# Kernel optimization log

Measured on AMD Instinct MI355X. Metric: run time of the kernel, lower is better.

The kernel has to match this reference:

```python
import jax, jax.numpy as jnp
import numpy as np

V_TH = 1.0
V_RESET = 0.0
BN_EPS = 1e-5

# Heaviside spike with ATan surrogate gradient (spikingjelly surrogate.ATan, alpha=2)
@jax.custom_vjp
def spike(x):
    return (x >= 0).astype(x.dtype)

def _spike_fwd(x):
    return spike(x), x

def _spike_bwd(x, g):
    alpha = 2.0
    sg = (alpha / 2.0) / (1.0 + (jnp.pi / 2.0 * alpha * x) ** 2)
    return (g * sg,)

spike.defvjp(_spike_fwd, _spike_bwd)


def lif_block(x, w, W, b, gamma, beta):
    """LTLIF (learnable tau, decay_input=False, hard reset) -> Linear -> BatchNorm1d.
    x: [T, B, C]"""
    inv_tau = jax.nn.sigmoid(w)  # 1/tau, learnable via w

    def step(v, xt):
        # decay_input=False charge: v = v - (v - v_reset)/tau + x_t
        v = v - (v - V_RESET) * inv_tau + xt
        s = spike(v - V_TH)
        v = (1.0 - s) * v + s * V_RESET  # hard reset
        return v, s

    v0 = jnp.full(x.shape[1:], V_RESET, dtype=x.dtype)
    _, spikes = jax.lax.scan(step, v0, x)  # spikes: [T, B, C]

    y = jnp.einsum('tbc,dc->tbd', spikes, W) + b  # Linear per step
    # BatchNorm1d in multi-step mode: stats over flattened (T*B) per channel
    mean = jnp.mean(y, axis=(0, 1))
    var = jnp.var(y, axis=(0, 1))
    y = (y - mean) * jax.lax.rsqrt(var + BN_EPS) * gamma + beta
    return y


def setup_inputs() -> dict:
    key = jax.random.key(0)
    ks = jax.random.split(key, 3)
    T, B, C = 128, 256, 512
    scale = 1.0 / np.sqrt(C)
    return {
        'x': jax.random.normal(ks[0], (T, B, C), jnp.float32),
        'w0': jnp.zeros((), jnp.float32),  # sigmoid(0)=0.5 => tau=2
        'W0': jax.random.normal(ks[1], (C, C), jnp.float32) * scale,
        'b0': jnp.zeros((C,), jnp.float32),
        'gamma0': jnp.ones((C,), jnp.float32),
        'beta0': jnp.zeros((C,), jnp.float32),
        'w1': jnp.zeros((), jnp.float32),
        'W1': jax.random.normal(ks[2], (C, C), jnp.float32) * scale,
        'b1': jnp.zeros((C,), jnp.float32),
        'gamma1': jnp.ones((C,), jnp.float32),
        'beta1': jnp.zeros((C,), jnp.float32),
    }


def reference(x, w0, W0, b0, gamma0, beta0, w1, W1, b1, gamma1, beta1):
    h = lif_block(x, w0, W0, b0, gamma0, beta0)   # process block (Dropout p=0 -> identity)
    h = lif_block(h, w1, W1, b1, gamma1, beta1)   # out block
    return h + x  # skip_connect=True
```

## Files before the change

kernel.cpp:

```cpp
#include <hip/hip_runtime.h>


typedef int i32x4 __attribute__((ext_vector_type(4)));

#define T_STEPS 128
#define BATCH   256
#define CH      512
#define BC      (BATCH * CH)
#define MROWS   (T_STEPS * BATCH)

__device__ __forceinline__ void llds16(const void* g, void* l) {
  __builtin_amdgcn_global_load_lds(
      (const __attribute__((address_space(1))) void*)g,
      (__attribute__((address_space(3))) void*)l, 16, 0, 0);
}

__global__ __launch_bounds__(256) void k_convw(const float* __restrict__ W0,
                                               const float* __restrict__ W1,
                                               signed char* __restrict__ WL0,
                                               signed char* __restrict__ WL1) {
  int b = blockIdx.x;
  const float* W = (b < 1024) ? W0 : W1;
  signed char* WL = (b < 1024) ? WL0 : WL1;
  int i = (b & 1023) * 256 + threadIdx.x;
  double z = (double)W[i] * 4294967296.0;
  z = fmin(fmax(z, -2147483647.0), 2147483647.0);
  int q = (int)llrint(z);
  int r = q;
  signed char l0 = (signed char)r; r = (r - l0) >> 8;
  signed char l1 = (signed char)r; r = (r - l1) >> 8;
  signed char l2 = (signed char)r; r = (r - l2) >> 8;
  signed char l3 = (signed char)r;
  WL[i]          = l0;
  WL[i + 262144] = l1;
  WL[i + 524288] = l2;
  WL[i + 786432] = l3;
}

__global__ __launch_bounds__(64) void k_lif1(const float* __restrict__ X,
                                             const float* __restrict__ wp,
                                             signed char* __restrict__ S) {
  int i = blockIdx.x * 64 + threadIdx.x;
  float om = 1.0f - 1.0f / (1.0f + expf(-wp[0]));
  float v = 0.0f;
  #pragma unroll 8
  for (int t = 0; t < T_STEPS; ++t) {
    float xt = X[(size_t)t * BC + i];
    v = v * om + xt;
    bool sp = (v >= 1.0f);
    S[(size_t)t * BC + i] = sp;
    v = sp ? 0.0f : v;
  }
}

__global__ __launch_bounds__(64) void k_lif2(const float* __restrict__ Y,
                                             const double* __restrict__ sA,
                                             const double* __restrict__ sB,
                                             const float* __restrict__ wp,
                                             signed char* __restrict__ S) {
  int i = blockIdx.x * 64 + threadIdx.x;
  int c = i & (CH - 1);
  double a = sA[c], b = sB[c];
  float om = 1.0f - 1.0f / (1.0f + expf(-wp[0]));
  float v = 0.0f;
  #pragma unroll 8
  for (int t = 0; t < T_STEPS; ++t) {
    float h = (float)((double)Y[(size_t)t * BC + i] * a + b);
    v = v * om + h;
    bool sp = (v >= 1.0f);
    S[(size_t)t * BC + i] = sp;
    v = sp ? 0.0f : v;
  }
}

__global__ __launch_bounds__(256) void k_gemm(const signed char* __restrict__ S,
                                              const signed char* __restrict__ WL,
                                              float* __restrict__ Y,
                                              double* __restrict__ sumP,
                                              double* __restrict__ sqP) {
  __shared__ __align__(16) signed char Bb[2][4][64 * 64];

  const int tid  = threadIdx.x;
  const int wid  = tid >> 6;
  const int lane = tid & 63;
  const int bid   = blockIdx.x;
  const int xcd   = bid & 7;
  const int local = bid >> 3;
  const int bn    = local & 7;
  const int bm    = xcd * 32 + (local >> 3);
  const int m0 = bm * 128, n0 = bn * 64;
  const int wm = wid >> 1, wn = wid & 1;
  const int lr = lane & 15, lg = lane >> 4;

  i32x4 acc[4][2][4] = {};

  auto STAGE = [&](int buf, int kt) {
    int row = tid >> 2, gl = tid & 3;
    int gg = gl ^ ((row >> 1) & 3);
    #pragma unroll
    for (int j = 0; j < 4; ++j)
      llds16(WL + (size_t)j * 262144 + (size_t)(n0 + row) * 512 + kt + gg * 16,
             (char*)Bb[buf][j] + wid * 1024);
  };

  const signed char* aP = S + (size_t)(m0 + wm * 64 + lr) * 512 + lg * 16;
  i32x4 a[2][4];

  STAGE(0, 0);
  #pragma unroll
  for (int m = 0; m < 4; ++m)
    a[0][m] = *(const i32x4*)(aP + m * 8192);

  #pragma unroll
  for (int i = 0; i < 8; ++i) {
    const int cur = i & 1;
    if (i < 7) {
      STAGE(cur ^ 1, (i + 1) * 64);
      #pragma unroll
      for (int m = 0; m < 4; ++m)
        a[cur ^ 1][m] = *(const i32x4*)(aP + m * 8192 + (i + 1) * 64);
    }
    if (i < 7) asm volatile("s_waitcnt vmcnt(8)" ::: "memory");
    else       asm volatile("s_waitcnt vmcnt(0)" ::: "memory");
    __builtin_amdgcn_s_barrier();
    asm volatile("" ::: "memory");

    i32x4 b[2][4];
    #pragma unroll
    for (int n = 0; n < 2; ++n) {
      int r = wn * 32 + n * 16 + lr;
      int g = lg ^ ((r >> 1) & 3);
      #pragma unroll
      for (int j = 0; j < 4; ++j)
        b[n][j] = *(const i32x4*)(Bb[cur][j] + r * 64 + g * 16);
    }
    __builtin_amdgcn_sched_barrier(0);

    __builtin_amdgcn_s_setprio(1);
    #pragma unroll
    for (int j = 0; j < 4; ++j)
      #pragma unroll
      for (int m = 0; m < 4; ++m)
        #pragma unroll
        for (int n = 0; n < 2; ++n)
          acc[m][n][j] = __builtin_amdgcn_mfma_i32_16x16x64_i8(
              a[cur][m], b[n][j], acc[m][n][j], 0, 0, 0);
    __builtin_amdgcn_s_setprio(0);

    asm volatile("s_waitcnt lgkmcnt(0)" ::: "memory");
    __builtin_amdgcn_s_barrier();
  }

  const int r0 = m0 + wm * 64 + lg * 4;
  const int cl = wn * 32 + lr;
  double s0 = 0, q0 = 0, s1 = 0, q1 = 0;
  #pragma unroll
  for (int m = 0; m < 4; ++m)
    #pragma unroll
    for (int n = 0; n < 2; ++n)
      #pragma unroll
      for (int q = 0; q < 4; ++q) {
        double yv = (((double)acc[m][n][3][q] * 256.0 + (double)acc[m][n][2][q]) * 256.0
                     + (double)acc[m][n][1][q]) * 256.0 + (double)acc[m][n][0][q];
        float yf = (float)(yv * 0x1p-32);
        Y[(size_t)(r0 + m * 16 + q) * 512 + n0 + cl + n * 16] = yf;
        double yd = (double)yf;
        if (n == 0) { s0 += yd; q0 += yd * yd; }
        else        { s1 += yd; q1 += yd * yd; }
      }
  s0 += __shfl_xor(s0, 16); s0 += __shfl_xor(s0, 32);
  q0 += __shfl_xor(q0, 16); q0 += __shfl_xor(q0, 32);
  s1 += __shfl_xor(s1, 16); s1 += __shfl_xor(s1, 32);
  q1 += __shfl_xor(q1, 16); q1 += __shfl_xor(q1, 32);

  double* shS = (double*)Bb[0][0];
  double* shQ = shS + 128;
  if (lane < 16) {
    shS[wm * 64 + cl]      = s0;  shQ[wm * 64 + cl]      = q0;
    shS[wm * 64 + cl + 16] = s1;  shQ[wm * 64 + cl + 16] = q1;
  }
  __syncthreads();
  if (tid < 64) {
    sumP[(size_t)(n0 + tid) * 256 + bm] = shS[tid] + shS[64 + tid];
    sqP [(size_t)(n0 + tid) * 256 + bm] = shQ[tid] + shQ[64 + tid];
  }
}

__global__ __launch_bounds__(256) void k_stats2(const double* __restrict__ sumP,
                                                const double* __restrict__ sqP,
                                                const float* __restrict__ gamma,
                                                const float* __restrict__ beta,
                                                double* __restrict__ sA,
                                                double* __restrict__ sB) {
  __shared__ double shS[256], shQ[256];
  int c = blockIdx.x;
  int t = threadIdx.x;
  shS[t] = sumP[(size_t)c * 256 + t];
  shQ[t] = sqP [(size_t)c * 256 + t];
  __syncthreads();
  for (int w = 128; w >= 1; w >>= 1) {
    if (t < w) { shS[t] += shS[t + w]; shQ[t] += shQ[t + w]; }
    __syncthreads();
  }
  if (t == 0) {
    const double invN = 1.0 / 32768.0;
    double mean = shS[0] * invN;
    double var  = shQ[0] * invN - mean * mean;
    double rstd = rsqrt(var + 1e-5);
    double a = (double)gamma[c] * rstd;
    sA[c] = a;
    sB[c] = (double)beta[c] - mean * a;
  }
}

__global__ __launch_bounds__(256) void k_final(float* __restrict__ Y,
                                               const float* __restrict__ X,
                                               const double* __restrict__ sA,
                                               const double* __restrict__ sB) {
  size_t i = (size_t)blockIdx.x * 256 + threadIdx.x;
  int c0 = (int)((i * 4) & (CH - 1));
  float4 y = ((const float4*)Y)[i];
  float4 x = ((const float4*)X)[i];
  float4 o;
  o.x = (float)((double)y.x * sA[c0 + 0] + sB[c0 + 0] + (double)x.x);
  o.y = (float)((double)y.y * sA[c0 + 1] + sB[c0 + 1] + (double)x.y);
  o.z = (float)((double)y.z * sA[c0 + 2] + sB[c0 + 2] + (double)x.z);
  o.w = (float)((double)y.w * sA[c0 + 3] + sB[c0 + 3] + (double)x.w);
  ((float4*)Y)[i] = o;
}

extern "C" void kernel_launch(void* const* d_in, const int* in_sizes, int n_in,
                              void* d_out, int out_size, void* d_ws, size_t ws_size,
                              hipStream_t stream) {
  (void)in_sizes; (void)n_in; (void)out_size; (void)ws_size;

  const float* x   = (const float*)d_in[0];
  const float* w0  = (const float*)d_in[1];
  const float* W0  = (const float*)d_in[2];
  const float* g0  = (const float*)d_in[4];
  const float* be0 = (const float*)d_in[5];
  const float* w1  = (const float*)d_in[6];
  const float* W1  = (const float*)d_in[7];
  const float* g1  = (const float*)d_in[9];
  const float* be1 = (const float*)d_in[10];
  float* Y = (float*)d_out;

  char* ws = (char*)d_ws;
  signed char* WL0  = (signed char*)(ws + 0x0000000);
  signed char* WL1  = (signed char*)(ws + 0x0100000);
  signed char* spk  = (signed char*)(ws + 0x0200000);
  double*      sumP = (double*)(ws + 0x1200000);
  double*      sqP  = (double*)(ws + 0x1300000);
  double*      sA   = (double*)(ws + 0x1400000);
  double*      sB   = (double*)(ws + 0x1402000);

  k_convw<<<2048, 256, 0, stream>>>(W0, W1, WL0, WL1);

  k_lif1 <<<BC / 64, 64, 0, stream>>>(x, w0, spk);
  k_gemm <<<(MROWS / 128) * (CH / 64), 256, 0, stream>>>(spk, WL0, Y, sumP, sqP);
  k_stats2<<<512, 256, 0, stream>>>(sumP, sqP, g0, be0, sA, sB);

  k_lif2 <<<BC / 64, 64, 0, stream>>>(Y, sA, sB, w1, spk);
  k_gemm <<<(MROWS / 128) * (CH / 64), 256, 0, stream>>>(spk, WL1, Y, sumP, sqP);
  k_stats2<<<512, 256, 0, stream>>>(sumP, sqP, g1, be1, sA, sB);

  k_final<<<(MROWS * CH) / (4 * 256), 256, 0, stream>>>(Y, x, sA, sB);
}
```

Before: 217.5 us.

## Drop LDS staging in int8 GEMM; each wave loads its own tiles directly

The GEMM kernel no longer stages weight tiles through shared memory with global_load_lds and barriers. Each wave now computes a 64x16 output tile and loads both A and B fragments straight from global memory into registers, with double buffering. The block tile shrinks to 64 rows, so the grid doubles, and the partial BN statistics are written per wave with a 512-wide stride that the stats kernel folds. This removes LDS traffic and barrier stalls and adds occupancy hints, at the cost of less data reuse and more redundant global and L2 reads of the spike and weight tiles.

```diff
diff --git a/kernel.cpp b/kernel.cpp
--- a/kernel.cpp
+++ b/kernel.cpp
@@ -8,12 +8,6 @@
 #define CH      512
 #define BC      (BATCH * CH)
 #define MROWS   (T_STEPS * BATCH)
-
-__device__ __forceinline__ void llds16(const void* g, void* l) {
-  __builtin_amdgcn_global_load_lds(
-      (const __attribute__((address_space(1))) void*)g,
-      (__attribute__((address_space(3))) void*)l, 16, 0, 0);
-}
 
 __global__ __launch_bounds__(256) void k_convw(const float* __restrict__ W0,
                                                const float* __restrict__ W1,
@@ -73,66 +67,46 @@
   }
 }
 
-__global__ __launch_bounds__(256) void k_gemm(const signed char* __restrict__ S,
-                                              const signed char* __restrict__ WL,
-                                              float* __restrict__ Y,
-                                              double* __restrict__ sumP,
-                                              double* __restrict__ sqP) {
-  __shared__ __align__(16) signed char Bb[2][4][64 * 64];
-
+__global__ __launch_bounds__(256, 3) void k_gemm(const signed char* __restrict__ S,
+                                                 const signed char* __restrict__ WL,
+                                                 float* __restrict__ Y,
+                                                 double* __restrict__ sumP,
+                                                 double* __restrict__ sqP) {
   const int tid  = threadIdx.x;
   const int wid  = tid >> 6;
   const int lane = tid & 63;
   const int bid   = blockIdx.x;
   const int xcd   = bid & 7;
   const int local = bid >> 3;
-  const int bn    = local & 7;
-  const int bm    = xcd * 32 + (local >> 3);
-  const int m0 = bm * 128, n0 = bn * 64;
-  const int wm = wid >> 1, wn = wid & 1;
+  const int bg    = local & 7;
+  const int bm    = xcd * 64 + (local >> 3);
+  const int m0 = bm * 64;
+  const int n0 = (bg * 4 + wid) * 16;
   const int lr = lane & 15, lg = lane >> 4;
 
-  i32x4 acc[4][2][4] = {};
-
-  auto STAGE = [&](int buf, int kt) {
-    int row = tid >> 2, gl = tid & 3;
-    int gg = gl ^ ((row >> 1) & 3);
-    #pragma unroll
-    for (int j = 0; j < 4; ++j)
-      llds16(WL + (size_t)j * 262144 + (size_t)(n0 + row) * 512 + kt + gg * 16,
-             (char*)Bb[buf][j] + wid * 1024);
-  };
-
-  const signed char* aP = S + (size_t)(m0 + wm * 64 + lr) * 512 + lg * 16;
-  i32x4 a[2][4];
-
-  STAGE(0, 0);
+  i32x4 acc[4][4] = {};
+
+  const signed char* aP = S  + (size_t)(m0 + lr) * 512 + lg * 16;
+  const signed char* bP = WL + (size_t)(n0 + lr) * 512 + lg * 16;
+
+  i32x4 aR[2][4], bR[2][4];
   #pragma unroll
   for (int m = 0; m < 4; ++m)
-    a[0][m] = *(const i32x4*)(aP + m * 8192);
+    aR[0][m] = *(const i32x4*)(aP + m * 8192);
+  #pragma unroll
+  for (int j = 0; j < 4; ++j)
+    bR[0][j] = *(const i32x4*)(bP + (size_t)j * 262144);
 
   #pragma unroll
   for (int i = 0; i < 8; ++i) {
-    const int cur = i & 1;
+    const int cur = i & 1, nxt = cur ^ 1;
     if (i < 7) {
-      STAGE(cur ^ 1, (i + 1) * 64);
       #pragma unroll
       for (int m = 0; m < 4; ++m)
-        a[cur ^ 1][m] = *(const i32x4*)(aP + m * 8192 + (i + 1) * 64);
-    }
-    if (i < 7) asm volatile("s_waitcnt vmcnt(8)" ::: "memory");
-    else       asm volatile("s_waitcnt vmcnt(0)" ::: "memory");
-    __builtin_amdgcn_s_barrier();
-    asm volatile("" ::: "memory");
-
-    i32x4 b[2][4];
-    #pragma unroll
-    for (int n = 0; n < 2; ++n) {
-      int r = wn * 32 + n * 16 + lr;
-      int g = lg ^ ((r >> 1) & 3);
+        aR[nxt][m] = *(const i32x4*)(aP + m * 8192 + (i + 1) * 64);
       #pragma unroll
       for (int j = 0; j < 4; ++j)
-        b[n][j] = *(const i32x4*)(Bb[cur][j] + r * 64 + g * 16);
+        bR[nxt][j] = *(const i32x4*)(bP + (size_t)j * 262144 + (i + 1) * 64);
     }
     __builtin_amdgcn_sched_barrier(0);
 
@@ -141,48 +115,29 @@
     for (int j = 0; j < 4; ++j)
       #pragma unroll
       for (int m = 0; m < 4; ++m)
-        #pragma unroll
-        for (int n = 0; n < 2; ++n)
-          acc[m][n][j] = __builtin_amdgcn_mfma_i32_16x16x64_i8(
-              a[cur][m], b[n][j], acc[m][n][j], 0, 0, 0);
+        acc[m][j] = __builtin_amdgcn_mfma_i32_16x16x64_i8(
+            aR[cur][m], bR[cur][j], acc[m][j], 0, 0, 0);
     __builtin_amdgcn_s_setprio(0);
-
-    asm volatile("s_waitcnt lgkmcnt(0)" ::: "memory");
-    __builtin_amdgcn_s_barrier();
-  }
-
-  const int r0 = m0 + wm * 64 + lg * 4;
-  const int cl = wn * 32 + lr;
-  double s0 = 0, q0 = 0, s1 = 0, q1 = 0;
+  }
+
+  const int r0 = m0 + lg * 4;
+  double s = 0, q = 0;
   #pragma unroll
   for (int m = 0; m < 4; ++m)
     #pragma unroll
-    for (int n = 0; n < 2; ++n)
-      #pragma unroll
-      for (int q = 0; q < 4; ++q) {
-        double yv = (((double)acc[m][n][3][q] * 256.0 + (double)acc[m][n][2][q]) * 256.0
-                     + (double)acc[m][n][1][q]) * 256.0 + (double)acc[m][n][0][q];
-        float yf = (float)(yv * 0x1p-32);
-        Y[(size_t)(r0 + m * 16 + q) * 512 + n0 + cl + n * 16] = yf;
-        double yd = (double)yf;
-        if (n == 0) { s0 += yd; q0 += yd * yd; }
-        else        { s1 += yd; q1 += yd * yd; }
-      }
-  s0 += __shfl_xor(s0, 16); s0 += __shfl_xor(s0, 32);
-  q0 += __shfl_xor(q0, 16); q0 += __shfl_xor(q0, 32);
-  s1 += __shfl_xor(s1, 16); s1 += __shfl_xor(s1, 32);
-  q1 += __shfl_xor(q1, 16); q1 += __shfl_xor(q1, 32);
-
-  double* shS = (double*)Bb[0][0];
-  double* shQ = shS + 128;
+    for (int qi = 0; qi < 4; ++qi) {
+      double yv = (((double)acc[m][3][qi] * 256.0 + (double)acc[m][2][qi]) * 256.0
+                   + (double)acc[m][1][qi]) * 256.0 + (double)acc[m][0][qi];
+      float yf = (float)(yv * 0x1p-32);
+      Y[(size_t)(r0 + m * 16 + qi) * 512 + n0 + lr] = yf;
+      double yd = (double)yf;
+      s += yd; q += yd * yd;
+    }
+  s += __shfl_xor(s, 16); s += __shfl_xor(s, 32);
+  q += __shfl_xor(q, 16); q += __shfl_xor(q, 32);
   if (lane < 16) {
-    shS[wm * 64 + cl]      = s0;  shQ[wm * 64 + cl]      = q0;
-    shS[wm * 64 + cl + 16] = s1;  shQ[wm * 64 + cl + 16] = q1;
-  }
-  __syncthreads();
-  if (tid < 64) {
-    sumP[(size_t)(n0 + tid) * 256 + bm] = shS[tid] + shS[64 + tid];
-    sqP [(size_t)(n0 + tid) * 256 + bm] = shQ[tid] + shQ[64 + tid];
+    sumP[(size_t)(n0 + lane) * 512 + bm] = s;
+    sqP [(size_t)(n0 + lane) * 512 + bm] = q;
   }
 }
 
@@ -195,8 +150,8 @@
   __shared__ double shS[256], shQ[256];
   int c = blockIdx.x;
   int t = threadIdx.x;
-  shS[t] = sumP[(size_t)c * 256 + t];
-  shQ[t] = sqP [(size_t)c * 256 + t];
+  shS[t] = sumP[(size_t)c * 512 + t] + sumP[(size_t)c * 512 + t + 256];
+  shQ[t] = sqP [(size_t)c * 512 + t] + sqP [(size_t)c * 512 + t + 256];
   __syncthreads();
   for (int w = 128; w >= 1; w >>= 1) {
     if (t < w) { shS[t] += shS[t + w]; shQ[t] += shQ[t + w]; }
@@ -250,18 +205,18 @@
   signed char* WL1  = (signed char*)(ws + 0x0100000);
   signed char* spk  = (signed char*)(ws + 0x0200000);
   double*      sumP = (double*)(ws + 0x1200000);
-  double*      sqP  = (double*)(ws + 0x1300000);
-  double*      sA   = (double*)(ws + 0x1400000);
-  double*      sB   = (double*)(ws + 0x1402000);
+  double*      sqP  = (double*)(ws + 0x1400000);
+  double*      sA   = (double*)(ws + 0x1600000);
+  double*      sB   = (double*)(ws + 0x1602000);
 
   k_convw<<<2048, 256, 0, stream>>>(W0, W1, WL0, WL1);
 
   k_lif1 <<<BC / 64, 64, 0, stream>>>(x, w0, spk);
-  k_gemm <<<(MROWS / 128) * (CH / 64), 256, 0, stream>>>(spk, WL0, Y, sumP, sqP);
+  k_gemm <<<(MROWS / 64) * (CH / 64), 256, 0, stream>>>(spk, WL0, Y, sumP, sqP);
   k_stats2<<<512, 256, 0, stream>>>(sumP, sqP, g0, be0, sA, sB);
 
   k_lif2 <<<BC / 64, 64, 0, stream>>>(Y, sA, sB, w1, spk);
-  k_gemm <<<(MROWS / 128) * (CH / 64), 256, 0, stream>>>(spk, WL1, Y, sumP, sqP);
+  k_gemm <<<(MROWS / 64) * (CH / 64), 256, 0, stream>>>(spk, WL1, Y, sumP, sqP);
   k_stats2<<<512, 256, 0, stream>>>(sumP, sqP, g1, be1, sA, sB);
 
   k_final<<<(MROWS * CH) / (4 * 256), 256, 0, stream>>>(Y, x, sA, sB);
```

Measured after the change: 312.4 us. 43.6% more time.
